# Optimization experiments

Hardware: AMD Instinct MI355X
Metric: run time of the kernel (lower is better)

Reference implementation:

```python
import jax, jax.numpy as jnp
import numpy as np

EPS = 1e-5

def _ln(x, g, b):
    mu = jnp.mean(x, axis=-1, keepdims=True)
    var = jnp.mean(jnp.square(x - mu), axis=-1, keepdims=True)
    return (x - mu) * jax.lax.rsqrt(var + EPS) * g + b


def setup_inputs() -> dict:
    key = jax.random.key(0)
    ks = jax.random.split(key, 16)
    B, T, D, H = 8, 4096, 512, 1024
    s_d = 1.0 / np.sqrt(D)
    s_h = 1.0 / np.sqrt(H)
    return {
        "x": jax.random.normal(ks[0], (B, T, D), dtype=jnp.float32),
        "gamma": jnp.ones((D,), jnp.float32),
        "beta": jnp.zeros((D,), jnp.float32),
        "Wq": jax.random.uniform(ks[1], (D, H), jnp.float32, -s_d, s_d),
        "bq": jax.random.uniform(ks[2], (H,), jnp.float32, -s_d, s_d),
        "Wk": jax.random.uniform(ks[3], (D, H), jnp.float32, -s_d, s_d),
        "bk": jax.random.uniform(ks[4], (H,), jnp.float32, -s_d, s_d),
        "Wv": jax.random.uniform(ks[5], (D, H), jnp.float32, -s_d, s_d),
        "bv": jax.random.uniform(ks[6], (H,), jnp.float32, -s_d, s_d),
        "wbias": jax.random.uniform(ks[7], (H,), jnp.float32, 0.0, 1.0),
        "Wo": jax.random.uniform(ks[8], (H, D), jnp.float32, -s_h, s_h),
        "bo": jax.random.uniform(ks[9], (D,), jnp.float32, -s_h, s_h),
        "W1": jax.random.uniform(ks[10], (D, H), jnp.float32, -s_d, s_d),
        "b1": jax.random.uniform(ks[11], (H,), jnp.float32, -s_d, s_d),
        "W2": jax.random.uniform(ks[12], (H, D), jnp.float32, -s_h, s_h),
        "b2": jax.random.uniform(ks[13], (D,), jnp.float32, -s_h, s_h),
    }


def reference(x, gamma, beta, Wq, bq, Wk, bk, Wv, bv, wbias, Wo, bo, W1, b1, W2, b2):
    # --- pre-LN ---
    x1 = _ln(x, gamma, beta)                      # [B,T,D]
    # --- AFTFull attention (NOTE: sums over BATCH dim 0, as in original repo) ---
    Q = jnp.einsum('btd,dh->bth', x1, Wq) + bq    # [B,T,H]
    K = jnp.einsum('btd,dh->bth', x1, Wk) + bk
    V = jnp.einsum('btd,dh->bth', x1, Wv) + bv
    Q_sig = jax.nn.sigmoid(Q)
    numer = jnp.exp(K + wbias)                    # [B,T,H]
    denom = jnp.sum(numer, axis=0)                # [T,H]
    weighted = jnp.sum(numer * V, axis=0) / denom # [T,H]
    Yt = Q_sig * weighted                         # [B,T,H] (broadcast)
    Yt = jnp.einsum('bth,hd->btd', Yt, Wo) + bo   # [B,T,D]
    x2 = Yt + x1                                  # residual (dropout = identity, eval)
    # --- second LN (same params, as in original) + MLP ---
    x3 = _ln(x2, gamma, beta)
    h = jax.nn.gelu(jnp.einsum('btd,dh->bth', x3, W1) + b1, approximate=False)
    m = jnp.einsum('bth,hd->btd', h, W2) + b2
    # original: out = dropout(m) + m  ==  2*m at eval (no residual to x2)
    return m + m
```

## Files before the change

kernel.cpp:

```cpp
#include <hip/hip_runtime.h>
#include <hip/hip_bf16.h>
#include <cstdint>

using u16 = unsigned short;
using u32 = unsigned int;

typedef __bf16 bf16x8 __attribute__((ext_vector_type(8)));
typedef float  f32x4  __attribute__((ext_vector_type(4)));

#define DEV static __device__ __forceinline__

DEV float bf2f(u16 u){ union { u32 u; float f; } c; c.u = ((u32)u) << 16; return c.f; }

DEV u16 f2bf(float f){
  __bf16 h = (__bf16)f;
  return __builtin_bit_cast(u16, h);
}

DEV float fast_rcp(float x){ return __builtin_amdgcn_rcpf(x); }

DEV void async16(const u16* g, u16* l){
  __builtin_amdgcn_global_load_lds((const __attribute__((address_space(1))) u32*)g,
                                   (__attribute__((address_space(3))) u32*)l,
                                   16, 0, 0);
}

#define BARRIER() do { __builtin_amdgcn_s_barrier(); \
                       __builtin_amdgcn_sched_barrier(0); } while (0)
#define LGKM0() do { __asm__ volatile("s_waitcnt lgkmcnt(0)" ::: "memory"); \
                     __builtin_amdgcn_sched_barrier(0); } while (0)
#define VMCNT(n) __asm__ volatile("s_waitcnt vmcnt(" #n ")" ::: "memory")

__global__ __launch_bounds__(256)
void transpose_all(const float* __restrict__ W0, const float* __restrict__ W1,
                   const float* __restrict__ W2, const float* __restrict__ W3,
                   const float* __restrict__ W4, const float* __restrict__ W5,
                   u16* __restrict__ T0, u16* __restrict__ T1, u16* __restrict__ T2,
                   u16* __restrict__ T3, u16* __restrict__ T4, u16* __restrict__ T5){
  const int z = blockIdx.z;
  const float* W; u16* WT; int R, C;
  switch (z){
    case 0:  W = W0; WT = T0; R = 512;  C = 1024; break;
    case 1:  W = W1; WT = T1; R = 512;  C = 1024; break;
    case 2:  W = W2; WT = T2; R = 512;  C = 1024; break;
    case 3:  W = W3; WT = T3; R = 1024; C = 512;  break;
    case 4:  W = W4; WT = T4; R = 512;  C = 1024; break;
    default: W = W5; WT = T5; R = 1024; C = 512;  break;
  }
  const int c0 = blockIdx.x * 32, r0 = blockIdx.y * 32;
  if (c0 >= C || r0 >= R) return;
  __shared__ float tile[32][33];
  const int tx = threadIdx.x, ty = threadIdx.y;
  #pragma unroll
  for (int j = 0; j < 4; ++j)
    tile[ty + j*8][tx] = W[(size_t)(r0 + ty + j*8) * C + (c0 + tx)];
  __syncthreads();
  #pragma unroll
  for (int j = 0; j < 4; ++j)
    WT[(size_t)(c0 + ty + j*8) * R + (r0 + tx)] = f2bf(tile[tx][ty + j*8]);
}

template<bool BF16IN>
__global__ __launch_bounds__(256)
void ln_kernel(const void* __restrict__ xin, const float* __restrict__ gamma,
               const float* __restrict__ beta, u16* __restrict__ xout){
  const int wid = threadIdx.x >> 6;
  const int lane = threadIdx.x & 63;
  const size_t row = (size_t)blockIdx.x * 4 + wid;
  const int d0 = lane * 8;
  float v[8];
  if constexpr (BF16IN){
    const u16* xp = (const u16*)xin + row * 512 + d0;
    uint4 p = *(const uint4*)xp;
    const u16* s = (const u16*)&p;
    #pragma unroll
    for (int i = 0; i < 8; ++i) v[i] = bf2f(s[i]);
  } else {
    const float* xp = (const float*)xin + row * 512 + d0;
    float4 p0 = *(const float4*)xp;
    float4 p1 = *(const float4*)(xp + 4);
    v[0]=p0.x; v[1]=p0.y; v[2]=p0.z; v[3]=p0.w;
    v[4]=p1.x; v[5]=p1.y; v[6]=p1.z; v[7]=p1.w;
  }
  float s = 0.f, sq = 0.f;
  #pragma unroll
  for (int i = 0; i < 8; ++i){ s += v[i]; sq += v[i]*v[i]; }
  #pragma unroll
  for (int o = 32; o >= 1; o >>= 1){ s += __shfl_xor(s, o); sq += __shfl_xor(sq, o); }
  const float mu  = s * (1.0f/512.0f);
  const float var = sq * (1.0f/512.0f) - mu*mu;
  const float rstd = rsqrtf(var + 1e-5f);
  const float4 g0 = *(const float4*)(gamma + d0);
  const float4 g1 = *(const float4*)(gamma + d0 + 4);
  const float4 b0 = *(const float4*)(beta + d0);
  const float4 b1 = *(const float4*)(beta + d0 + 4);
  float gg[8] = {g0.x,g0.y,g0.z,g0.w,g1.x,g1.y,g1.z,g1.w};
  float bb[8] = {b0.x,b0.y,b0.z,b0.w,b1.x,b1.y,b1.z,b1.w};
  u16 o8[8];
  #pragma unroll
  for (int i = 0; i < 8; ++i)
    o8[i] = f2bf((v[i]-mu)*rstd*gg[i] + bb[i]);
  *(uint4*)(xout + row*512 + d0) = *(const uint4*)o8;
}

__global__ __launch_bounds__(256)
void aft_fused(const u16* __restrict__ numer, const u16* __restrict__ V,
               const u16* __restrict__ qs, u16* __restrict__ yt){
  const size_t TH = (size_t)4096 * 1024;
  const size_t i8 = ((size_t)blockIdx.x * 256 + threadIdx.x) * 8;
  float den[8], ws[8];
  #pragma unroll
  for (int j = 0; j < 8; ++j){ den[j] = 0.f; ws[j] = 0.f; }
  #pragma unroll
  for (int b = 0; b < 8; ++b){
    uint4 pn = *(const uint4*)(numer + b*TH + i8);
    uint4 pv = *(const uint4*)(V     + b*TH + i8);
    const u16* n = (const u16*)&pn;
    const u16* v = (const u16*)&pv;
    #pragma unroll
    for (int j = 0; j < 8; ++j){ float nf = bf2f(n[j]); den[j] += nf; ws[j] += nf * bf2f(v[j]); }
  }
  float w[8];
  #pragma unroll
  for (int j = 0; j < 8; ++j) w[j] = ws[j] * fast_rcp(den[j]);
  #pragma unroll
  for (int b = 0; b < 8; ++b){
    uint4 pq = *(const uint4*)(qs + b*TH + i8);
    const u16* q = (const u16*)&pq;
    u16 o[8];
    #pragma unroll
    for (int j = 0; j < 8; ++j) o[j] = f2bf(bf2f(q[j]) * w[j]);
    *(uint4*)(yt + b*TH + i8) = *(const uint4*)o;
  }
}

template<int EPI, int KC>
__global__ __launch_bounds__(512, 2)
void gemm256(const u16* __restrict__ A, const u16* __restrict__ Bt,
             const float* __restrict__ bias0, const float* __restrict__ wbias,
             u16* __restrict__ out0, u16* __restrict__ out1, u16* __restrict__ out2,
             const float* __restrict__ bias1, const float* __restrict__ bias2,
             const u16* __restrict__ resid, float* __restrict__ outf){
  constexpr int NKS = KC / 32;
  __shared__ __align__(16) char smem[65536];

  const int tid  = threadIdx.x;
  const int wid  = tid >> 6;
  const int lane = tid & 63;
  const int quad = lane >> 4;
  const int lr   = lane & 15;
  const int wm   = wid & 1;
  const int wn   = wid >> 1;

  const int nwg = gridDim.x;
  const int wg  = (blockIdx.x & 7) * (nwg >> 3) + (blockIdx.x >> 3);
  const int nNT = nwg >> 7;
  const int sgs = nNT << 2;
  const int sg  = wg / sgs;
  const int r   = wg - sg * sgs;
  const int tileM = (sg*4 + (r & 3)) * 256;
  const int tileN = (r >> 2) * 256;

  const u16 *pA0, *pA1, *pB0, *pB1;
  {
    const int o0 = tid << 4;
    const int r0_ = o0 >> 6,          c0_ = (o0 >> 4) & 3;
    const int r1_ = (o0 + 8192) >> 6, c1_ = c0_;
    pA0 = A  + (size_t)(tileM + r0_) * KC + (c0_ ^ ((r0_ >> 1) & 3)) * 8;
    pA1 = A  + (size_t)(tileM + r1_) * KC + (c1_ ^ ((r1_ >> 1) & 3)) * 8;
    pB0 = Bt + (size_t)(tileN + r0_) * KC + (c0_ ^ ((r0_ >> 1) & 3)) * 8;
    pB1 = Bt + (size_t)(tileN + r1_) * KC + (c1_ ^ ((r1_ >> 1) & 3)) * 8;
  }
  auto stageA = [&](char* nb, int kt){
    char* d = nb + wid*1024 + (lane << 4);
    async16(pA0 + kt, (u16*)d);
    async16(pA1 + kt, (u16*)(d + 8192));
  };
  auto stageB = [&](char* nb, int kt){
    char* d = nb + 16384 + wid*1024 + (lane << 4);
    async16(pB0 + kt, (u16*)d);
    async16(pB1 + kt, (u16*)(d + 8192));
  };

  int aOff[2][4], bOff[2][2];
  #pragma unroll
  for (int mh = 0; mh < 2; ++mh)
    #pragma unroll
    for (int i = 0; i < 4; ++i){
      const int rw = wm*128 + mh*64 + i*16 + lr;
      aOff[mh][i] = rw*64 + ((quad ^ ((rw >> 1) & 3)) << 4);
    }
  #pragma unroll
  for (int nh = 0; nh < 2; ++nh)
    #pragma unroll
    for (int j = 0; j < 2; ++j){
      const int rw = wn*64 + nh*32 + j*16 + lr;
      bOff[nh][j] = 16384 + rw*64 + ((quad ^ ((rw >> 1) & 3)) << 4);
    }

  bf16x8 ar[4], br[2][2];
  f32x4 acc[2][2][4][2] = {};

  auto ldA = [&](const char* cb, int mh){
    #pragma unroll
    for (int i = 0; i < 4; ++i) ar[i] = *(const bf16x8*)(cb + aOff[mh][i]);
  };
  auto ldB = [&](const char* cb){
    #pragma unroll
    for (int nh = 0; nh < 2; ++nh)
      #pragma unroll
      for (int j = 0; j < 2; ++j) br[nh][j] = *(const bf16x8*)(cb + bOff[nh][j]);
  };
  auto MF = [&](int mh){
    __builtin_amdgcn_s_setprio(1);
    #pragma unroll
    for (int i = 0; i < 4; ++i)
      #pragma unroll
      for (int nh = 0; nh < 2; ++nh)
        #pragma unroll
        for (int j = 0; j < 2; ++j)
          acc[mh][nh][i][j] = __builtin_amdgcn_mfma_f32_16x16x32_bf16(br[nh][j], ar[i], acc[mh][nh][i][j], 0, 0, 0);
    __builtin_amdgcn_s_setprio(0);
  };

  stageA(smem, 0); stageB(smem, 0);
  VMCNT(0);
  BARRIER();

  #pragma unroll 1
  for (int t = 0; t < NKS-1; ++t){
    const char* cb = smem + (t & 1)*32768;
    char* nb = smem + ((t & 1) ^ 1)*32768;
    const int kt = (t + 1) << 5;
    stageA(nb, kt);
    ldA(cb, 0); ldB(cb);
    LGKM0();
    MF(0);
    stageB(nb, kt);
    ldA(cb, 1);
    LGKM0();
    MF(1);
    VMCNT(0);
    BARRIER();
  }
  {
    const char* cb = smem + ((NKS-1) & 1)*32768;
    ldA(cb, 0); ldB(cb);
    LGKM0();
    MF(0);
    ldA(cb, 1);
    LGKM0();
    MF(1);
  }

  if (EPI == 3){
    #pragma unroll
    for (int mh = 0; mh < 2; ++mh)
    #pragma unroll
    for (int i = 0; i < 4; ++i){
      const int row = tileM + wm*128 + mh*64 + i*16 + lr;
      #pragma unroll
      for (int nh = 0; nh < 2; ++nh)
      #pragma unroll
      for (int j = 0; j < 2; ++j){
        const int colb = tileN + wn*64 + nh*32 + j*16 + quad*4;
        const float4 bvv = *(const float4*)(bias0 + colb);
        float4 o;
        #pragma unroll
        for (int r_ = 0; r_ < 4; ++r_)
          ((float*)&o)[r_] = 2.0f * (acc[mh][nh][i][j][r_] + ((const float*)&bvv)[r_]);
        *(float4*)(outf + (size_t)row * 512 + colb) = o;
      }
    }
    return;
  }

  BARRIER();
  char* eb = smem + wid * 2304;
  const int mat = (EPI == 0) ? (tileN >> 10) : 0;
  const float* biasP = bias0;
  u16* outP = out0;
  int ldO = 1024, cb0 = tileN + wn*64;
  if (EPI == 0){
    biasP = (mat==0) ? bias0 : (mat==1) ? bias1 : bias2;
    outP  = (mat==0) ? out0  : (mat==1) ? out1  : out2;
    cb0   = (tileN & 1023) + wn*64;
  } else if (EPI == 1){
    ldO = 512;
  }

  #pragma unroll
  for (int mh = 0; mh < 2; ++mh)
  #pragma unroll
  for (int i = 0; i < 4; ++i){
    const int row = tileM + wm*128 + mh*64 + i*16 + lr;
    #pragma unroll
    for (int nh = 0; nh < 2; ++nh)
    #pragma unroll
    for (int j = 0; j < 2; ++j){
      const int cl = (nh*2 + j)*16 + quad*4;
      const float4 bvv = *(const float4*)(biasP + cb0 + cl);
      u16 o[4];
      if (EPI == 0){
        float4 wbv = {0,0,0,0};
        if (mat == 1) wbv = *(const float4*)(wbias + cb0 + cl);
        #pragma unroll
        for (int r_ = 0; r_ < 4; ++r_){
          float v = acc[mh][nh][i][j][r_] + ((const float*)&bvv)[r_];
          if (mat == 0)      v = fast_rcp(1.0f + __expf(-v));
          else if (mat == 1) v = __expf(v + ((const float*)&wbv)[r_]);
          o[r_] = f2bf(v);
        }
      } else if (EPI == 1){
        uint2 pr = *(const uint2*)(resid + (size_t)row * 512 + cb0 + cl);
        const u16* rp = (const u16*)&pr;
        #pragma unroll
        for (int r_ = 0; r_ < 4; ++r_)
          o[r_] = f2bf(acc[mh][nh][i][j][r_] + ((const float*)&bvv)[r_] + bf2f(rp[r_]));
      } else {
        #pragma unroll
        for (int r_ = 0; r_ < 4; ++r_){
          float v  = acc[mh][nh][i][j][r_] + ((const float*)&bvv)[r_];
          float u2 = 2.0f * v * (0.7978845608f + 0.0356774081f * v * v);
          float tg = 1.0f - 2.0f * fast_rcp(1.0f + __expf(u2));
          o[r_] = f2bf(0.5f * v * (1.0f + tg));
        }
      }
      *(uint2*)(eb + lr*144 + cl*2) = *(const uint2*)o;
    }
    __asm__ volatile("s_waitcnt lgkmcnt(0)" ::: "memory");
    uint4 p0 = *(const uint4*)(eb + lr*144 + quad*32);
    uint4 p1 = *(const uint4*)(eb + lr*144 + quad*32 + 16);
    __asm__ volatile("s_waitcnt lgkmcnt(0)" ::: "memory");
    u16* gp = outP + (size_t)row * ldO + cb0 + quad*16;
    *(uint4*)gp = p0;
    *(uint4*)(gp + 8) = p1;
  }
}

extern "C" void kernel_launch(void* const* d_in, const int* in_sizes, int n_in,
                              void* d_out, int out_size, void* d_ws, size_t ws_size,
                              hipStream_t stream) {
  const float* x     = (const float*)d_in[0];
  const float* gamma = (const float*)d_in[1];
  const float* beta  = (const float*)d_in[2];
  const float* Wq    = (const float*)d_in[3];
  const float* bq    = (const float*)d_in[4];
  const float* Wk    = (const float*)d_in[5];
  const float* bk    = (const float*)d_in[6];
  const float* Wv    = (const float*)d_in[7];
  const float* bv    = (const float*)d_in[8];
  const float* wbias = (const float*)d_in[9];
  const float* Wo    = (const float*)d_in[10];
  const float* bo    = (const float*)d_in[11];
  const float* W1    = (const float*)d_in[12];
  const float* b1    = (const float*)d_in[13];
  const float* W2    = (const float*)d_in[14];
  const float* b2    = (const float*)d_in[15];
  float* out = (float*)d_out;

  char* w = (char*)d_ws;
  const size_t MB = 1ull << 20;
  u16* WqkvT = (u16*)(w + 0*MB);
  u16* WoT   = (u16*)(w + 3*MB);
  u16* W1T   = (u16*)(w + 4*MB);
  u16* W2T   = (u16*)(w + 5*MB);
  u16* x1b   = (u16*)(w + 6*MB);
  u16* Qs    = (u16*)(w + 38*MB);
  u16* Nu    = (u16*)(w + 102*MB);
  u16* Vb    = (u16*)(w + 166*MB);
  u16* Yt    = Nu;
  u16* x2b   = Vb;
  u16* x3b   = (u16*)(w + 198*MB);
  u16* hb    = Qs;

  transpose_all<<<dim3(32, 32, 6), dim3(32, 8), 0, stream>>>(
      Wq, Wk, Wv, Wo, W1, W2,
      WqkvT, WqkvT + 1024*512, WqkvT + 2*1024*512, WoT, W1T, W2T);

  ln_kernel<false><<<8192, 256, 0, stream>>>(x, gamma, beta, x1b);

  gemm256<0, 512><<<1536, 512, 0, stream>>>(x1b, WqkvT,
      bq, wbias, Qs, Nu, Vb, bk, bv, nullptr, nullptr);

  aft_fused<<<2048, 256, 0, stream>>>(Nu, Vb, Qs, Yt);

  gemm256<1, 1024><<<256, 512, 0, stream>>>(Yt, WoT,
      bo, nullptr, x2b, nullptr, nullptr, nullptr, nullptr, x1b, nullptr);

  ln_kernel<true><<<8192, 256, 0, stream>>>(x2b, gamma, beta, x3b);

  gemm256<2, 512><<<512, 512, 0, stream>>>(x3b, W1T,
      b1, nullptr, hb, nullptr, nullptr, nullptr, nullptr, nullptr, nullptr);

  gemm256<3, 1024><<<256, 512, 0, stream>>>(hb, W2T,
      b2, nullptr, nullptr, nullptr, nullptr, nullptr, nullptr, nullptr, out);
}
```

Before: 490.5 us.

## Load B fragments straight to registers and stage only A through LDS

Restructures the bf16 GEMM main loop to use a 64-wide K step. Only the A tile is staged into LDS, with a new XOR swizzle. B fragments are loaded directly from global memory into double-buffered registers one step ahead, which halves LDS traffic and the LDS reads of B. The cost is redundant global/L2 reads of B across waves that share columns, higher register pressure, and removal of the barrier before the epilogue, which relies on the last iteration using the upper LDS buffer.

Result: slower. 573.0 us (+16.8%).

```diff
diff --git a/kernel.cpp b/kernel.cpp
--- a/kernel.cpp
+++ b/kernel.cpp
@@ -25,11 +25,10 @@
                                    16, 0, 0);
 }
 
-#define BARRIER() do { __builtin_amdgcn_s_barrier(); \
-                       __builtin_amdgcn_sched_barrier(0); } while (0)
-#define LGKM0() do { __asm__ volatile("s_waitcnt lgkmcnt(0)" ::: "memory"); \
-                     __builtin_amdgcn_sched_barrier(0); } while (0)
-#define VMCNT(n) __asm__ volatile("s_waitcnt vmcnt(" #n ")" ::: "memory")
+#define SB() __builtin_amdgcn_sched_barrier(0)
+#define BARRIER() do { __builtin_amdgcn_s_barrier(); SB(); } while (0)
+#define LGKM0() do { __asm__ volatile("s_waitcnt lgkmcnt(0)" ::: "memory"); SB(); } while (0)
+#define VMCNT0() do { __asm__ volatile("s_waitcnt vmcnt(0)" ::: "memory"); SB(); } while (0)
 
 __global__ __launch_bounds__(256)
 void transpose_all(const float* __restrict__ W0, const float* __restrict__ W1,
@@ -141,7 +140,7 @@
              u16* __restrict__ out0, u16* __restrict__ out1, u16* __restrict__ out2,
              const float* __restrict__ bias1, const float* __restrict__ bias2,
              const u16* __restrict__ resid, float* __restrict__ outf){
-  constexpr int NKS = KC / 32;
+  constexpr int NT = KC / 64;
   __shared__ __align__(16) char smem[65536];
 
   const int tid  = threadIdx.x;
@@ -161,96 +160,80 @@
   const int tileM = (sg*4 + (r & 3)) * 256;
   const int tileN = (r >> 2) * 256;
 
-  const u16 *pA0, *pA1, *pB0, *pB1;
-  {
-    const int o0 = tid << 4;
-    const int r0_ = o0 >> 6,          c0_ = (o0 >> 4) & 3;
-    const int r1_ = (o0 + 8192) >> 6, c1_ = c0_;
-    pA0 = A  + (size_t)(tileM + r0_) * KC + (c0_ ^ ((r0_ >> 1) & 3)) * 8;
-    pA1 = A  + (size_t)(tileM + r1_) * KC + (c1_ ^ ((r1_ >> 1) & 3)) * 8;
-    pB0 = Bt + (size_t)(tileN + r0_) * KC + (c0_ ^ ((r0_ >> 1) & 3)) * 8;
-    pB1 = Bt + (size_t)(tileN + r1_) * KC + (c1_ ^ ((r1_ >> 1) & 3)) * 8;
-  }
+  const u16* pA = A + (size_t)(tileM + wid*32 + (lane >> 3)) * KC
+                    + (((lane & 7) ^ (lane >> 3)) << 3);
   auto stageA = [&](char* nb, int kt){
-    char* d = nb + wid*1024 + (lane << 4);
-    async16(pA0 + kt, (u16*)d);
-    async16(pA1 + kt, (u16*)(d + 8192));
-  };
-  auto stageB = [&](char* nb, int kt){
-    char* d = nb + 16384 + wid*1024 + (lane << 4);
-    async16(pB0 + kt, (u16*)d);
-    async16(pB1 + kt, (u16*)(d + 8192));
-  };
-
-  int aOff[2][4], bOff[2][2];
-  #pragma unroll
-  for (int mh = 0; mh < 2; ++mh)
-    #pragma unroll
-    for (int i = 0; i < 4; ++i){
-      const int rw = wm*128 + mh*64 + i*16 + lr;
-      aOff[mh][i] = rw*64 + ((quad ^ ((rw >> 1) & 3)) << 4);
-    }
+    char* d = nb + wid*4096 + (lane << 4);
+    #pragma unroll
+    for (int rr = 0; rr < 4; ++rr)
+      async16(pA + (size_t)rr*8*KC + kt, (u16*)(d + rr*1024));
+  };
+
+  const u16* pB[2][2];
   #pragma unroll
   for (int nh = 0; nh < 2; ++nh)
     #pragma unroll
-    for (int j = 0; j < 2; ++j){
-      const int rw = wn*64 + nh*32 + j*16 + lr;
-      bOff[nh][j] = 16384 + rw*64 + ((quad ^ ((rw >> 1) & 3)) << 4);
-    }
-
-  bf16x8 ar[4], br[2][2];
+    for (int j = 0; j < 2; ++j)
+      pB[nh][j] = Bt + (size_t)(tileN + wn*64 + nh*32 + j*16 + lr) * KC + quad*8;
+
+  const int cO0 = ((quad)     ^ (lr & 7)) << 4;
+  const int cO1 = ((quad ^ 4) ^ (lr & 7)) << 4;
+  const int aRowBase = (wm*128 + lr) * 128;
+
+  bf16x8 ar[4][2];
+  bf16x8 brA[2][2][2], brB[2][2][2];
   f32x4 acc[2][2][4][2] = {};
 
-  auto ldA = [&](const char* cb, int mh){
-    #pragma unroll
-    for (int i = 0; i < 4; ++i) ar[i] = *(const bf16x8*)(cb + aOff[mh][i]);
-  };
-  auto ldB = [&](const char* cb){
+  auto loadB = [&](bf16x8 (&br)[2][2][2], int kt){
     #pragma unroll
     for (int nh = 0; nh < 2; ++nh)
       #pragma unroll
-      for (int j = 0; j < 2; ++j) br[nh][j] = *(const bf16x8*)(cb + bOff[nh][j]);
-  };
-  auto MF = [&](int mh){
+      for (int j = 0; j < 2; ++j){
+        br[nh][j][0] = *(const bf16x8*)(pB[nh][j] + kt);
+        br[nh][j][1] = *(const bf16x8*)(pB[nh][j] + kt + 32);
+      }
+  };
+  auto ldA = [&](const char* cb, int mh){
+    #pragma unroll
+    for (int i = 0; i < 4; ++i){
+      ar[i][0] = *(const bf16x8*)(cb + aRowBase + mh*8192 + i*2048 + cO0);
+      ar[i][1] = *(const bf16x8*)(cb + aRowBase + mh*8192 + i*2048 + cO1);
+    }
+  };
+  auto MF = [&](int mh, bf16x8 (&br)[2][2][2]){
     __builtin_amdgcn_s_setprio(1);
     #pragma unroll
     for (int i = 0; i < 4; ++i)
       #pragma unroll
       for (int nh = 0; nh < 2; ++nh)
         #pragma unroll
-        for (int j = 0; j < 2; ++j)
-          acc[mh][nh][i][j] = __builtin_amdgcn_mfma_f32_16x16x32_bf16(br[nh][j], ar[i], acc[mh][nh][i][j], 0, 0, 0);
+        for (int j = 0; j < 2; ++j){
+          acc[mh][nh][i][j] = __builtin_amdgcn_mfma_f32_16x16x32_bf16(br[nh][j][0], ar[i][0], acc[mh][nh][i][j], 0, 0, 0);
+          acc[mh][nh][i][j] = __builtin_amdgcn_mfma_f32_16x16x32_bf16(br[nh][j][1], ar[i][1], acc[mh][nh][i][j], 0, 0, 0);
+        }
     __builtin_amdgcn_s_setprio(0);
   };
 
-  stageA(smem, 0); stageB(smem, 0);
-  VMCNT(0);
-  BARRIER();
-
-  #pragma unroll 1
-  for (int t = 0; t < NKS-1; ++t){
-    const char* cb = smem + (t & 1)*32768;
-    char* nb = smem + ((t & 1) ^ 1)*32768;
-    const int kt = (t + 1) << 5;
-    stageA(nb, kt);
-    ldA(cb, 0); ldB(cb);
+  loadB(brA, 0);
+  stageA(smem, 0);
+
+  auto step = [&](const char* cb, char* nb,
+                  bf16x8 (&brCur)[2][2][2], bf16x8 (&brNxt)[2][2][2], int t){
+    VMCNT0();
+    BARRIER();
+    ldA(cb, 0);
     LGKM0();
-    MF(0);
-    stageB(nb, kt);
+    if (t + 1 < NT){ loadB(brNxt, (t+1)*64); stageA(nb, (t+1)*64); }
+    MF(0, brCur);
     ldA(cb, 1);
     LGKM0();
-    MF(1);
-    VMCNT(0);
-    BARRIER();
-  }
-  {
-    const char* cb = smem + ((NKS-1) & 1)*32768;
-    ldA(cb, 0); ldB(cb);
-    LGKM0();
-    MF(0);
-    ldA(cb, 1);
-    LGKM0();
-    MF(1);
+    MF(1, brCur);
+  };
+
+  #pragma unroll 1
+  for (int t = 0; t < NT; t += 2){
+    step(smem,         smem + 32768, brA, brB, t);
+    step(smem + 32768, smem,         brB, brA, t + 1);
   }
 
   if (EPI == 3){
@@ -275,7 +258,6 @@
     return;
   }
 
-  BARRIER();
   char* eb = smem + wid * 2304;
   const int mat = (EPI == 0) ? (tileN >> 10) : 0;
   const float* biasP = bias0;
```
